# Optimization experiments

Hardware: AMD Instinct MI355X
Metric: run time of the kernel (lower is better)

The kernel has to match this reference:

```python
import jax, jax.numpy as jnp
import numpy as np

ALPHA = 0.2  # LeakyReLU negative slope
NEG_INF = -9e15


def setup_inputs() -> dict:
    key = jax.random.key(0)
    k1, k2, k3, k4, k5 = jax.random.split(key, 5)
    B, N, D = 4, 4096, 256
    feat = jax.random.normal(k1, (B, N, D), dtype=jnp.float32)
    adj = jax.random.randint(k2, (B, N, N), 0, 2, dtype=jnp.int32)
    W = jax.random.normal(k3, (D, D), dtype=jnp.float32) * (1.414 / np.sqrt(D))
    a_1 = jax.random.normal(k4, (D, 1), dtype=jnp.float32) * 0.1
    a_2 = jax.random.normal(k5, (D, 1), dtype=jnp.float32) * 0.1
    return {"feat": feat, "adj": adj, "W": W, "a_1": a_1, "a_2": a_2}


def reference(feat, adj, W, a_1, a_2):
    # h: [B, N, D]
    h = jnp.matmul(feat, W)
    Ax = jnp.matmul(h, a_1)  # [B, N, 1]
    Ay = jnp.matmul(h, a_2)  # [B, N, 1]
    # logits[b, i, j] = Ax[b, j] + Ay[b, i]
    logits = jnp.swapaxes(Ax, 1, 2) + Ay  # [B, N, N]
    e = jax.nn.leaky_relu(logits, negative_slope=ALPHA)
    e = jnp.where(adj > 0, e, jnp.float32(NEG_INF))
    attention = jax.nn.softmax(e, axis=-1)  # dropout p=0.0 -> identity
    h_prime = jnp.matmul(attention, feat)  # [B, N, in_features]
    h_out = jnp.matmul(h_prime, W)  # [B, N, out_features]
    return jax.nn.elu(h_out)
```

## Files before the change

### kernel.cpp

```cpp
#include <hip/hip_runtime.h>

typedef __attribute__((ext_vector_type(8))) short short8;
typedef __attribute__((ext_vector_type(4))) float f32x4;
typedef __attribute__((ext_vector_type(4))) int i32x4;

#define LOG2E 1.44269504f
#define FT_STRIDE 4128
#define FT_BATCH (256 * FT_STRIDE)

__device__ __forceinline__ short f2bf(float f) {
  unsigned u = __builtin_bit_cast(unsigned, f);
  u += 0x7fffu + ((u >> 16) & 1u);
  return (short)(u >> 16);
}

__global__ void gat_wvec(const float* __restrict__ W, const float* __restrict__ a1,
                         const float* __restrict__ a2, float* __restrict__ w1,
                         float* __restrict__ w2) {
  __shared__ float a1f[256], a2f[256];
  const int tid = threadIdx.x;
  a1f[tid] = a1[tid];
  a2f[tid] = a2[tid];
  __syncthreads();
  float s1 = 0.f, s2 = 0.f;
  const float4* wr = (const float4*)(W + (size_t)tid * 256);
  for (int d0 = 0; d0 < 64; ++d0) {
    float4 v = wr[d0];
    s1 += v.x * a1f[d0 * 4] + v.y * a1f[d0 * 4 + 1] + v.z * a1f[d0 * 4 + 2] + v.w * a1f[d0 * 4 + 3];
    s2 += v.x * a2f[d0 * 4] + v.y * a2f[d0 * 4 + 1] + v.z * a2f[d0 * 4 + 2] + v.w * a2f[d0 * 4 + 3];
  }
  w1[tid] = s1;
  w2[tid] = s2;
}

__global__ void convT(const float* __restrict__ src, short* __restrict__ dst,
                      int R, int C, int dstStride, size_t dstBatch) {
  __shared__ short T[64][72];
  const int tid = threadIdx.x;
  const int bc = blockIdx.x, br = blockIdx.y, bb = blockIdx.z;
  const float* s = src + (size_t)bb * R * C;
  short* d = dst + (size_t)bb * dstBatch;
  const int rr = tid >> 2, cc = (tid & 3) << 4;
  const float4* sp = (const float4*)(s + (size_t)(br * 64 + rr) * C + bc * 64 + cc);
  alignas(16) short v[16];
#pragma unroll
  for (int g = 0; g < 4; ++g) {
    float4 x = sp[g];
    v[g * 4 + 0] = f2bf(x.x);
    v[g * 4 + 1] = f2bf(x.y);
    v[g * 4 + 2] = f2bf(x.z);
    v[g * 4 + 3] = f2bf(x.w);
  }
  *(short8*)&T[rr][cc] = *(short8*)&v[0];
  *(short8*)&T[rr][cc + 8] = *(short8*)&v[8];
  __syncthreads();
#pragma unroll
  for (int j = 0; j < 16; ++j) v[j] = T[cc + j][rr];
  short8* dp = (short8*)(d + (size_t)(bc * 64 + rr) * dstStride + br * 64 + cc);
  dp[0] = *(short8*)&v[0];
  dp[1] = *(short8*)&v[8];
}

__global__ void gat_axay(const float* __restrict__ feat, const float* __restrict__ w1,
                         const float* __restrict__ w2, float* __restrict__ AxL,
                         float* __restrict__ AyL) {
  const int lane = threadIdx.x & 63;
  const int row = blockIdx.x * 4 + (threadIdx.x >> 6);
  float4 fv = *(const float4*)(feat + (size_t)row * 256 + lane * 4);
  const float4 w1v = *(const float4*)(w1 + lane * 4);
  const float4 w2v = *(const float4*)(w2 + lane * 4);
  float s1 = fv.x * w1v.x + fv.y * w1v.y + fv.z * w1v.z + fv.w * w1v.w;
  float s2 = fv.x * w2v.x + fv.y * w2v.y + fv.z * w2v.z + fv.w * w2v.w;
#pragma unroll
  for (int off = 32; off >= 1; off >>= 1) {
    s1 += __shfl_xor(s1, off);
    s2 += __shfl_xor(s2, off);
  }
  if (lane == 0) { AxL[row] = s1 * LOG2E; AyL[row] = s2 * LOG2E; }
}

__global__ void gat_max(const float* __restrict__ AxL, float* __restrict__ MbL) {
  __shared__ float red[256];
  const int b = blockIdx.x, tid = threadIdx.x;
  float m = -3.4e38f;
  for (int i = tid; i < 4096; i += 256) m = fmaxf(m, AxL[b * 4096 + i]);
  red[tid] = m;
  __syncthreads();
  for (int s = 128; s > 0; s >>= 1) {
    if (tid < s) red[tid] = fmaxf(red[tid], red[tid + s]);
    __syncthreads();
  }
  if (tid == 0) MbL[b] = m = red[0];
}

__global__ __launch_bounds__(512, 4) void gat_attn(
    const short* __restrict__ featT,
    const int* __restrict__ adj,
    const float* __restrict__ AxL, const float* __restrict__ AyL,
    const float* __restrict__ MbL,
    const short* __restrict__ WT,
    float* __restrict__ out)
{
  __shared__ short smem[8704];

  const int tid = threadIdx.x;
  const int blk = blockIdx.x;
  const int x = blk & 7;
  const int b = x >> 1;
  const int it = ((blk >> 3) << 1) | (x & 1);
  const int i0 = it << 5;

  const int r = tid >> 4;
  const int cg = tid & 15;

  const float ayL = AyL[b * 4096 + i0 + r];
  const float sL = ayL + MbL[b];
  const float mrL = fmaxf(sL, 0.2f * sL);
  const float aL = ayL - mrL;
  const float dd = -0.8f * mrL;

  const int lane = tid & 63;
  const int w = tid >> 6;
  const int n0 = w << 5;
  const int l15 = lane & 15;
  const int q = lane >> 4;

  f32x4 acc[2][2], lac[2];
#pragma unroll
  for (int i = 0; i < 2; ++i) {
    lac[i] = (f32x4){0.f, 0.f, 0.f, 0.f};
#pragma unroll
    for (int j = 0; j < 2; ++j) acc[i][j] = (f32x4){0.f, 0.f, 0.f, 0.f};
  }

  short8 ones;
#pragma unroll
  for (int j = 0; j < 8; ++j) ones[j] = (short)0x3F80;

  const i32x4* adjp = (const i32x4*)(adj + ((size_t)(b * 4096 + i0 + r)) * 4096) + cg * 2;
  const float4* axp = (const float4*)(AxL + b * 4096) + cg * 2;
  const short* ftb = featT + ((size_t)b * FT_BATCH) + (size_t)(n0 + l15) * FT_STRIDE + q * 8;

  i32x4 adv[2];
  float4 axv[2];
  adv[0] = __builtin_nontemporal_load(adjp);
  adv[1] = __builtin_nontemporal_load(adjp + 1);
  axv[0] = axp[0];
  axv[1] = axp[1];

  for (int jc = 0; jc < 32; ++jc) {
    const int buf = (jc & 1) * 4352;
    unsigned pw[4];
#pragma unroll
    for (int g = 0; g < 2; ++g) {
      const float* af = (const float*)&axv[g];
      unsigned pr[4];
#pragma unroll
      for (int u = 0; u < 4; ++u) {
        float v = af[u] + aL;
        float uu = fmaxf(v, fmaf(0.2f, v, dd));
        unsigned ub = adv[g][u] > 0 ? __builtin_bit_cast(unsigned, uu) : 0xFF800000u;
        float p = __builtin_amdgcn_exp2f(__builtin_bit_cast(float, ub));
        pr[u] = __builtin_bit_cast(unsigned, p) + 0x8000u;
      }
      pw[g * 2]     = __builtin_amdgcn_perm(pr[1], pr[0], 0x07060302u);
      pw[g * 2 + 1] = __builtin_amdgcn_perm(pr[3], pr[2], 0x07060302u);
    }
    *(uint4*)(smem + buf + r * 136 + cg * 8) = *(uint4*)pw;
    __syncthreads();

    if (jc < 31) {
      adv[0] = __builtin_nontemporal_load(adjp + (jc + 1) * 32);
      adv[1] = __builtin_nontemporal_load(adjp + (jc + 1) * 32 + 1);
      axv[0] = axp[(jc + 1) * 32];
      axv[1] = axp[(jc + 1) * 32 + 1];
    }

    const int j0 = jc << 7;
#pragma unroll
    for (int k0 = 0; k0 < 128; k0 += 32) {
      short8 a0 = *(const short8*)(smem + buf + l15 * 136 + k0 + q * 8);
      short8 a1 = *(const short8*)(smem + buf + (16 + l15) * 136 + k0 + q * 8);
      lac[0] = __builtin_amdgcn_mfma_f32_16x16x32_bf16(a0, ones, lac[0], 0, 0, 0);
      lac[1] = __builtin_amdgcn_mfma_f32_16x16x32_bf16(a1, ones, lac[1], 0, 0, 0);
#pragma unroll
      for (int ct = 0; ct < 2; ++ct) {
        short8 bfr = *(const short8*)(ftb + (size_t)ct * 16 * FT_STRIDE + j0 + k0);
        acc[0][ct] = __builtin_amdgcn_mfma_f32_16x16x32_bf16(a0, bfr, acc[0][ct], 0, 0, 0);
        acc[1][ct] = __builtin_amdgcn_mfma_f32_16x16x32_bf16(a1, bfr, acc[1][ct], 0, 0, 0);
      }
    }
  }

  float linv[2][4];
#pragma unroll
  for (int rt = 0; rt < 2; ++rt)
#pragma unroll
    for (int reg = 0; reg < 4; ++reg) {
      float l = lac[rt][reg];
      linv[rt][reg] = l > 0.f ? 1.f / l : 0.f;
    }

  __syncthreads();
  short* hbuf = smem;
#pragma unroll
  for (int rt = 0; rt < 2; ++rt)
#pragma unroll
    for (int reg = 0; reg < 4; ++reg) {
      const int lr = rt * 16 + q * 4 + reg;
#pragma unroll
      for (int ct = 0; ct < 2; ++ct)
        hbuf[lr * 264 + n0 + ct * 16 + l15] = f2bf(acc[rt][ct][reg] * linv[rt][reg]);
    }
  __syncthreads();

  f32x4 ac2[2][2];
#pragma unroll
  for (int i = 0; i < 2; ++i)
#pragma unroll
    for (int j = 0; j < 2; ++j) ac2[i][j] = (f32x4){0.f, 0.f, 0.f, 0.f};

#pragma unroll 2
  for (int k0 = 0; k0 < 256; k0 += 32) {
    short8 afr0 = *(const short8*)&hbuf[l15 * 264 + k0 + q * 8];
    short8 afr1 = *(const short8*)&hbuf[(16 + l15) * 264 + k0 + q * 8];
#pragma unroll
    for (int ct = 0; ct < 2; ++ct) {
      short8 bfr = *(const short8*)(WT + (size_t)(n0 + ct * 16 + l15) * 256 + k0 + q * 8);
      ac2[0][ct] = __builtin_amdgcn_mfma_f32_16x16x32_bf16(afr0, bfr, ac2[0][ct], 0, 0, 0);
      ac2[1][ct] = __builtin_amdgcn_mfma_f32_16x16x32_bf16(afr1, bfr, ac2[1][ct], 0, 0, 0);
    }
  }

#pragma unroll
  for (int rt = 0; rt < 2; ++rt)
#pragma unroll
    for (int reg = 0; reg < 4; ++reg) {
      const int row = i0 + rt * 16 + q * 4 + reg;
      float* orow = out + ((size_t)(b * 4096 + row)) * 256 + n0 + l15;
#pragma unroll
      for (int ct = 0; ct < 2; ++ct) {
        float v = ac2[rt][ct][reg];
        float o = v > 0.f ? v : (__builtin_amdgcn_exp2f(v * LOG2E) - 1.f);
        __builtin_nontemporal_store(o, orow + ct * 16);
      }
    }
}

extern "C" void kernel_launch(void* const* d_in, const int* in_sizes, int n_in,
                              void* d_out, int out_size, void* d_ws, size_t ws_size,
                              hipStream_t stream) {
  (void)in_sizes; (void)n_in; (void)out_size; (void)ws_size;
  const float* feat = (const float*)d_in[0];
  const int* adj = (const int*)d_in[1];
  const float* W = (const float*)d_in[2];
  const float* a1 = (const float*)d_in[3];
  const float* a2 = (const float*)d_in[4];
  float* out = (float*)d_out;

  char* ws = (char*)d_ws;
  short* featT   = (short*)ws;
  short* WT      = (short*)(ws + 8454144);
  float* AxL     = (float*)(ws + 8585216);
  float* AyL     = (float*)(ws + 8650752);
  float* MbL     = (float*)(ws + 8716288);
  float* w1      = (float*)(ws + 8717312);
  float* w2      = (float*)(ws + 8718336);

  hipLaunchKernelGGL(gat_wvec, dim3(1), dim3(256), 0, stream, W, a1, a2, w1, w2);
  hipLaunchKernelGGL(convT, dim3(4, 4, 1), dim3(256), 0, stream, W, WT, 256, 256, 256, (size_t)65536);
  hipLaunchKernelGGL(convT, dim3(4, 64, 4), dim3(256), 0, stream, feat, featT, 4096, 256, FT_STRIDE, (size_t)FT_BATCH);
  hipLaunchKernelGGL(gat_axay, dim3(4096), dim3(256), 0, stream, feat, w1, w2, AxL, AyL);
  hipLaunchKernelGGL(gat_max, dim3(4), dim3(256), 0, stream, AxL, MbL);
  hipLaunchKernelGGL(gat_attn, dim3(512), dim3(512), 0, stream, featT, adj, AxL, AyL, MbL, WT, out);
}
```

Measured before the change: 476.3 us.

## Stage featT tiles in swizzled LDS and remap waves to 16x64 output tiles

The attention kernel now stages each 64-column chunk of transposed features into double-buffered LDS with an XOR swizzle, instead of every wave reading its B fragments straight from global memory. Waves are remapped from 32 rows by 32 columns to 16 rows by 64 columns, and the j-chunk shrinks from 128 to 64 over 64 iterations. This is meant to cut redundant global and L2 traffic for featT and avoid LDS bank conflicts. In exchange LDS use grows to about 73 KB per block, which may limit occupancy against the launch bound of 4 blocks of 512 threads, and registers rise from prefetching four feature vectors.

Result: faster. 466.6 us (-2.0%).

```diff
diff --git a/kernel.cpp b/kernel.cpp
--- a/kernel.cpp
+++ b/kernel.cpp
@@ -3,6 +3,7 @@
 typedef __attribute__((ext_vector_type(8))) short short8;
 typedef __attribute__((ext_vector_type(4))) float f32x4;
 typedef __attribute__((ext_vector_type(4))) int i32x4;
+typedef __attribute__((ext_vector_type(2))) unsigned u32x2;
 
 #define LOG2E 1.44269504f
 #define FT_STRIDE 4128
@@ -90,7 +91,7 @@
     if (tid < s) red[tid] = fmaxf(red[tid], red[tid + s]);
     __syncthreads();
   }
-  if (tid == 0) MbL[b] = m = red[0];
+  if (tid == 0) MbL[b] = red[0];
 }
 
 __global__ __launch_bounds__(512, 4) void gat_attn(
@@ -101,7 +102,7 @@
     const short* __restrict__ WT,
     float* __restrict__ out)
 {
-  __shared__ short smem[8704];
+  __shared__ short smem[37376];
 
   const int tid = threadIdx.x;
   const int blk = blockIdx.x;
@@ -110,141 +111,142 @@
   const int it = ((blk >> 3) << 1) | (x & 1);
   const int i0 = it << 5;
 
-  const int r = tid >> 4;
-  const int cg = tid & 15;
-
-  const float ayL = AyL[b * 4096 + i0 + r];
+  const int pi = tid >> 4;
+  const int pj = tid & 15;
+  const float ayL = AyL[b * 4096 + i0 + pi];
   const float sL = ayL + MbL[b];
   const float mrL = fmaxf(sL, 0.2f * sL);
   const float aL = ayL - mrL;
   const float dd = -0.8f * mrL;
 
+  const int sn = tid >> 3;
+  const int so = tid & 7;
+  const int sph = ((so ^ (sn & 7)) << 3);
+
   const int lane = tid & 63;
   const int w = tid >> 6;
-  const int n0 = w << 5;
+  const int rowg = (w & 1) << 4;
+  const int colg = (w >> 1) << 6;
   const int l15 = lane & 15;
   const int q = lane >> 4;
-
-  f32x4 acc[2][2], lac[2];
-#pragma unroll
-  for (int i = 0; i < 2; ++i) {
-    lac[i] = (f32x4){0.f, 0.f, 0.f, 0.f};
-#pragma unroll
-    for (int j = 0; j < 2; ++j) acc[i][j] = (f32x4){0.f, 0.f, 0.f, 0.f};
-  }
+  const int swz = l15 & 7;
+  const int bu0 = (q ^ swz) << 3;
+  const int bu1 = ((q + 4) ^ swz) << 3;
+
+  f32x4 acc[4], lac;
+  lac = (f32x4){0.f, 0.f, 0.f, 0.f};
+#pragma unroll
+  for (int j = 0; j < 4; ++j) acc[j] = (f32x4){0.f, 0.f, 0.f, 0.f};
 
   short8 ones;
 #pragma unroll
   for (int j = 0; j < 8; ++j) ones[j] = (short)0x3F80;
 
-  const i32x4* adjp = (const i32x4*)(adj + ((size_t)(b * 4096 + i0 + r)) * 4096) + cg * 2;
-  const float4* axp = (const float4*)(AxL + b * 4096) + cg * 2;
-  const short* ftb = featT + ((size_t)b * FT_BATCH) + (size_t)(n0 + l15) * FT_STRIDE + q * 8;
-
-  i32x4 adv[2];
-  float4 axv[2];
-  adv[0] = __builtin_nontemporal_load(adjp);
-  adv[1] = __builtin_nontemporal_load(adjp + 1);
-  axv[0] = axp[0];
-  axv[1] = axp[1];
-
-  for (int jc = 0; jc < 32; ++jc) {
-    const int buf = (jc & 1) * 4352;
-    unsigned pw[4];
-#pragma unroll
-    for (int g = 0; g < 2; ++g) {
-      const float* af = (const float*)&axv[g];
+  const i32x4* adjp = (const i32x4*)(adj + ((size_t)(b * 4096 + i0 + pi)) * 4096) + pj;
+  const float4* axp = (const float4*)(AxL + b * 4096) + pj;
+  const short* ftb = featT + (size_t)b * FT_BATCH + (size_t)sn * FT_STRIDE + so * 8;
+
+  i32x4 adv;
+  float4 axv;
+  short8 bv[4];
+  adv = __builtin_nontemporal_load(adjp);
+  axv = axp[0];
+#pragma unroll
+  for (int k = 0; k < 4; ++k) bv[k] = *(const short8*)(ftb + (size_t)k * 64 * FT_STRIDE);
+
+  for (int jc = 0; jc < 64; ++jc) {
+    const int pb = jc & 1;
+    {
+      const float* af = (const float*)&axv;
       unsigned pr[4];
 #pragma unroll
       for (int u = 0; u < 4; ++u) {
         float v = af[u] + aL;
         float uu = fmaxf(v, fmaf(0.2f, v, dd));
-        unsigned ub = adv[g][u] > 0 ? __builtin_bit_cast(unsigned, uu) : 0xFF800000u;
+        unsigned ub = adv[u] > 0 ? __builtin_bit_cast(unsigned, uu) : 0xFF800000u;
         float p = __builtin_amdgcn_exp2f(__builtin_bit_cast(float, ub));
         pr[u] = __builtin_bit_cast(unsigned, p) + 0x8000u;
       }
-      pw[g * 2]     = __builtin_amdgcn_perm(pr[1], pr[0], 0x07060302u);
-      pw[g * 2 + 1] = __builtin_amdgcn_perm(pr[3], pr[2], 0x07060302u);
-    }
-    *(uint4*)(smem + buf + r * 136 + cg * 8) = *(uint4*)pw;
+      u32x2 pw;
+      pw[0] = __builtin_amdgcn_perm(pr[1], pr[0], 0x07060302u);
+      pw[1] = __builtin_amdgcn_perm(pr[3], pr[2], 0x07060302u);
+      *(u32x2*)(smem + 32768 + pb * 2304 + pi * 72 + pj * 4) = pw;
+    }
+    {
+      short* bs = smem + pb * 16384;
+#pragma unroll
+      for (int k = 0; k < 4; ++k)
+        *(short8*)(bs + (sn + 64 * k) * 64 + sph) = bv[k];
+    }
     __syncthreads();
 
-    if (jc < 31) {
-      adv[0] = __builtin_nontemporal_load(adjp + (jc + 1) * 32);
-      adv[1] = __builtin_nontemporal_load(adjp + (jc + 1) * 32 + 1);
-      axv[0] = axp[(jc + 1) * 32];
-      axv[1] = axp[(jc + 1) * 32 + 1];
-    }
-
-    const int j0 = jc << 7;
-#pragma unroll
-    for (int k0 = 0; k0 < 128; k0 += 32) {
-      short8 a0 = *(const short8*)(smem + buf + l15 * 136 + k0 + q * 8);
-      short8 a1 = *(const short8*)(smem + buf + (16 + l15) * 136 + k0 + q * 8);
-      lac[0] = __builtin_amdgcn_mfma_f32_16x16x32_bf16(a0, ones, lac[0], 0, 0, 0);
-      lac[1] = __builtin_amdgcn_mfma_f32_16x16x32_bf16(a1, ones, lac[1], 0, 0, 0);
-#pragma unroll
-      for (int ct = 0; ct < 2; ++ct) {
-        short8 bfr = *(const short8*)(ftb + (size_t)ct * 16 * FT_STRIDE + j0 + k0);
-        acc[0][ct] = __builtin_amdgcn_mfma_f32_16x16x32_bf16(a0, bfr, acc[0][ct], 0, 0, 0);
-        acc[1][ct] = __builtin_amdgcn_mfma_f32_16x16x32_bf16(a1, bfr, acc[1][ct], 0, 0, 0);
+    if (jc < 63) {
+      adv = __builtin_nontemporal_load(adjp + (jc + 1) * 16);
+      axv = axp[(jc + 1) * 16];
+#pragma unroll
+      for (int k = 0; k < 4; ++k)
+        bv[k] = *(const short8*)(ftb + (size_t)k * 64 * FT_STRIDE + (jc + 1) * 64);
+    }
+
+    const short* pbuf = smem + 32768 + pb * 2304;
+    const short* bsr = smem + pb * 16384;
+#pragma unroll
+    for (int h = 0; h < 2; ++h) {
+      const int k0 = h * 32;
+      const int bu = h ? bu1 : bu0;
+      short8 a = *(const short8*)(pbuf + (rowg + l15) * 72 + k0 + q * 8);
+      lac = __builtin_amdgcn_mfma_f32_16x16x32_bf16(a, ones, lac, 0, 0, 0);
+#pragma unroll
+      for (int ct = 0; ct < 4; ++ct) {
+        short8 bf = *(const short8*)(bsr + (colg + ct * 16 + l15) * 64 + bu);
+        acc[ct] = __builtin_amdgcn_mfma_f32_16x16x32_bf16(a, bf, acc[ct], 0, 0, 0);
       }
     }
   }
 
-  float linv[2][4];
-#pragma unroll
-  for (int rt = 0; rt < 2; ++rt)
-#pragma unroll
-    for (int reg = 0; reg < 4; ++reg) {
-      float l = lac[rt][reg];
-      linv[rt][reg] = l > 0.f ? 1.f / l : 0.f;
-    }
+  float linv[4];
+#pragma unroll
+  for (int reg = 0; reg < 4; ++reg) {
+    float l = lac[reg];
+    linv[reg] = l > 0.f ? 1.f / l : 0.f;
+  }
 
   __syncthreads();
   short* hbuf = smem;
 #pragma unroll
-  for (int rt = 0; rt < 2; ++rt)
-#pragma unroll
-    for (int reg = 0; reg < 4; ++reg) {
-      const int lr = rt * 16 + q * 4 + reg;
-#pragma unroll
-      for (int ct = 0; ct < 2; ++ct)
-        hbuf[lr * 264 + n0 + ct * 16 + l15] = f2bf(acc[rt][ct][reg] * linv[rt][reg]);
-    }
-  __syncthreads();
-
-  f32x4 ac2[2][2];
-#pragma unroll
-  for (int i = 0; i < 2; ++i)
-#pragma unroll
-    for (int j = 0; j < 2; ++j) ac2[i][j] = (f32x4){0.f, 0.f, 0.f, 0.f};
+  for (int reg = 0; reg < 4; ++reg) {
+    const int lr = rowg + q * 4 + reg;
+#pragma unroll
+    for (int ct = 0; ct < 4; ++ct)
+      hbuf[lr * 264 + colg + ct * 16 + l15] = f2bf(acc[ct][reg] * linv[reg]);
+  }
+  __syncthreads();
+
+  f32x4 ac2[4];
+#pragma unroll
+  for (int j = 0; j < 4; ++j) ac2[j] = (f32x4){0.f, 0.f, 0.f, 0.f};
 
 #pragma unroll 2
   for (int k0 = 0; k0 < 256; k0 += 32) {
-    short8 afr0 = *(const short8*)&hbuf[l15 * 264 + k0 + q * 8];
-    short8 afr1 = *(const short8*)&hbuf[(16 + l15) * 264 + k0 + q * 8];
-#pragma unroll
-    for (int ct = 0; ct < 2; ++ct) {
-      short8 bfr = *(const short8*)(WT + (size_t)(n0 + ct * 16 + l15) * 256 + k0 + q * 8);
-      ac2[0][ct] = __builtin_amdgcn_mfma_f32_16x16x32_bf16(afr0, bfr, ac2[0][ct], 0, 0, 0);
-      ac2[1][ct] = __builtin_amdgcn_mfma_f32_16x16x32_bf16(afr1, bfr, ac2[1][ct], 0, 0, 0);
-    }
-  }
-
-#pragma unroll
-  for (int rt = 0; rt < 2; ++rt)
-#pragma unroll
-    for (int reg = 0; reg < 4; ++reg) {
-      const int row = i0 + rt * 16 + q * 4 + reg;
-      float* orow = out + ((size_t)(b * 4096 + row)) * 256 + n0 + l15;
-#pragma unroll
-      for (int ct = 0; ct < 2; ++ct) {
-        float v = ac2[rt][ct][reg];
-        float o = v > 0.f ? v : (__builtin_amdgcn_exp2f(v * LOG2E) - 1.f);
-        __builtin_nontemporal_store(o, orow + ct * 16);
-      }
-    }
+    short8 a = *(const short8*)&hbuf[(rowg + l15) * 264 + k0 + q * 8];
+#pragma unroll
+    for (int ct = 0; ct < 4; ++ct) {
+      short8 bf = *(const short8*)(WT + (size_t)(colg + ct * 16 + l15) * 256 + k0 + q * 8);
+      ac2[ct] = __builtin_amdgcn_mfma_f32_16x16x32_bf16(a, bf, ac2[ct], 0, 0, 0);
+    }
+  }
+
+#pragma unroll
+  for (int reg = 0; reg < 4; ++reg) {
+    const int row = i0 + rowg + q * 4 + reg;
+    float* orow = out + ((size_t)(b * 4096 + row)) * 256 + colg + l15;
+#pragma unroll
+    for (int ct = 0; ct < 4; ++ct) {
+      float v = ac2[ct][reg];
+      float o = v > 0.f ? v : (__builtin_amdgcn_exp2f(v * LOG2E) - 1.f);
+      __builtin_nontemporal_store(o, orow + ct * 16);
+    }
+  }
 }
 
 extern "C" void kernel_launch(void* const* d_in, const int* in_sizes, int n_in,
```
